# Kernel optimization log

Measured on AMD Instinct MI355X. Metric: run time of the kernel, lower is better.

## Reference

```python
import jax, jax.numpy as jnp
import numpy as np

N_NODES = 10000
N_EDGES = 160000
HIDDEN = 64
NUM_RBF = 32
Q_DIM = 8
CUTOFF_UPPER = 5.0


def silu(x):
    return x * jax.nn.sigmoid(x)


def tensor_norm(X):
    # X: [n, 3, 3, H] -> [n, H] (Frobenius norm squared over the 3x3 dims)
    return (X * X).sum(axis=(1, 2))


def decompose_tensor(X):
    # X: [n, 3, 3, H] -> I: [n, H] (trace/3), A: antisym [n,3,3,H], S: sym traceless [n,3,3,H]
    eye = jnp.eye(3, dtype=X.dtype)[None, :, :, None]
    I = jnp.einsum('naah->nh', X) / 3.0
    Xt = X.transpose(0, 2, 1, 3)
    A = 0.5 * (X - Xt)
    S = 0.5 * (X + Xt) - I[:, None, None, :] * eye
    return I, A, S


def compose_tensor(I, A, S):
    eye = jnp.eye(3, dtype=A.dtype)[None, :, :, None]
    return I[:, None, None, :] * eye + A + S


def tmm(P, Q):
    # 3x3 matmul per (atom, channel): [n,3,3,H] x [n,3,3,H] -> [n,3,3,H]
    return jnp.einsum('nach,ncbh->nabh', P, Q)


def setup_inputs() -> dict:
    key = jax.random.key(0)
    ks = jax.random.split(key, 16)
    H = HIDDEN
    inp = {
        'X': jax.random.normal(ks[0], (N_NODES, 3, 3, H), jnp.float32),
        'charges': jax.random.normal(ks[1], (N_NODES, Q_DIM), jnp.float32),
        'edge_weight': jax.random.uniform(ks[2], (N_EDGES,), jnp.float32) * CUTOFF_UPPER,
        'edge_attr': jax.random.normal(ks[3], (N_EDGES, NUM_RBF), jnp.float32),
        'edge_index': jax.random.randint(ks[4], (2, N_EDGES), 0, N_NODES, jnp.int32),
    }
    d_in = NUM_RBF + 2 * Q_DIM
    inp['Ws1'] = jax.random.normal(ks[5], (d_in, H), jnp.float32) / np.sqrt(d_in).astype(np.float32)
    inp['bs1'] = jnp.zeros((H,), jnp.float32)
    inp['Ws2'] = jax.random.normal(ks[6], (H, 2 * H), jnp.float32) / np.sqrt(H).astype(np.float32)
    inp['bs2'] = jnp.zeros((2 * H,), jnp.float32)
    inp['Ws3'] = jax.random.normal(ks[7], (2 * H, 3 * H), jnp.float32) / np.sqrt(2 * H).astype(np.float32)
    inp['bs3'] = jnp.zeros((3 * H,), jnp.float32)
    for i in range(6):
        inp['Wt%d' % i] = jax.random.normal(ks[8 + i], (H, H), jnp.float32) / np.sqrt(H).astype(np.float32)
    return inp


def reference(X, charges, edge_weight, edge_attr, Ws1, bs1, Ws2, bs2, Ws3, bs3,
              Wt0, Wt1, Wt2, Wt3, Wt4, Wt5, edge_index):
    H = HIDDEN
    n = X.shape[0]
    row, col = edge_index[0], edge_index[1]
    # cosine cutoff (cutoff_lower = 0)
    C = 0.5 * (jnp.cos(edge_weight * (jnp.pi / CUTOFF_UPPER)) + 1.0)
    C = C * (edge_weight < CUTOFF_UPPER).astype(X.dtype)
    # edge scalar MLP on [rbf, q_i, q_j]
    h = jnp.concatenate([edge_attr, charges[row], charges[col]], axis=-1)
    h = silu(h @ Ws1 + bs1)
    h = silu(h @ Ws2 + bs2)
    h = silu(h @ Ws3 + bs3)
    w = (h * C[:, None]).reshape(h.shape[0], 3, H)  # [E, 3, H]
    # normalize node tensors
    X = X / (tensor_norm(X) + 1.0)[:, None, None, :]
    I, A, S = decompose_tensor(X)
    I = I @ Wt0
    A = A @ Wt1
    S = S @ Wt2
    Y = compose_tensor(I, A, S)
    # message passing: gather I/A/S at source (edge_index[1]), weight per component, scatter-add at dest (edge_index[0])
    eye = jnp.eye(3, dtype=X.dtype)[None, :, :, None]
    msg_e = ((w[:, 0] * I[col])[:, None, None, :] * eye
             + w[:, 1][:, None, None, :] * A[col]
             + w[:, 2][:, None, None, :] * S[col])  # [E, 3, 3, H]
    msg = jax.ops.segment_sum(msg_e, row, num_segments=n)  # [n, 3, 3, H]
    # O(3): C = msg @ Y + Y @ msg (3x3 matmul per channel)
    Cm = tmm(msg, Y) + tmm(Y, msg)
    I2, A2, S2 = decompose_tensor(Cm)
    normp1 = tensor_norm(Cm) + 1.0
    I2 = I2 / normp1
    A2 = A2 / normp1[:, None, None, :]
    S2 = S2 / normp1[:, None, None, :]
    I2 = I2 @ Wt3
    A2 = A2 @ Wt4
    S2 = S2 @ Wt5
    dX = compose_tensor(I2, A2, S2)
    return X + dX + tmm(dX, dX)
```

## Files before the change

kernel.cpp:

```cpp
#include <hip/hip_runtime.h>
#include <math.h>

#define HD 64

typedef _Float16 half8 __attribute__((ext_vector_type(8)));
typedef _Float16 half4v __attribute__((ext_vector_type(4)));
typedef float floatx4 __attribute__((ext_vector_type(4)));

__device__ __forceinline__ float silu_f(float x) {
    return x * __builtin_amdgcn_rcpf(1.0f + __expf(-x));
}

__global__ __launch_bounds__(256) void node_pre(
    const float* __restrict__ X,
    const float* __restrict__ Wt0, const float* __restrict__ Wt1, const float* __restrict__ Wt2,
    float* __restrict__ Tn, _Float16* __restrict__ TnH, int N)
{
    int sub = threadIdx.x >> 6;
    int h = threadIdx.x & 63;
    int n = blockIdx.x * 4 + sub;
    int nn = (n < N) ? n : (N - 1);

    const float* Xb = X + (size_t)nn * 9 * HD + h;
    float x[9];
    float nrm = 0.f;
#pragma unroll
    for (int i = 0; i < 9; ++i) { x[i] = Xb[i * HD]; nrm += x[i] * x[i]; }
    float inv = 1.0f / (nrm + 1.0f);
#pragma unroll
    for (int i = 0; i < 9; ++i) x[i] *= inv;

    float I0 = (x[0] + x[4] + x[8]) * (1.0f / 3.0f);
    __shared__ float comp[4][10][HD];
    comp[sub][0][h] = I0;
    comp[sub][1][h] = 0.5f * (x[1] - x[3]);
    comp[sub][2][h] = 0.5f * (x[2] - x[6]);
    comp[sub][3][h] = 0.5f * (x[5] - x[7]);
    comp[sub][4][h] = x[0] - I0;
    comp[sub][5][h] = 0.5f * (x[1] + x[3]);
    comp[sub][6][h] = 0.5f * (x[2] + x[6]);
    comp[sub][7][h] = x[4] - I0;
    comp[sub][8][h] = 0.5f * (x[5] + x[7]);
    comp[sub][9][h] = x[8] - I0;
    __syncthreads();
    float acc[10];
#pragma unroll
    for (int i = 0; i < 10; ++i) acc[i] = 0.f;
    for (int k = 0; k < HD; ++k) {
        float w0 = Wt0[k * HD + h];
        float w1 = Wt1[k * HD + h];
        float w2 = Wt2[k * HD + h];
        acc[0] += comp[sub][0][k] * w0;
        acc[1] += comp[sub][1][k] * w1;
        acc[2] += comp[sub][2][k] * w1;
        acc[3] += comp[sub][3][k] * w1;
#pragma unroll
        for (int j = 0; j < 6; ++j) acc[4 + j] += comp[sub][4 + j][k] * w2;
    }
    if (n < N) {
        float* tp = Tn + (size_t)n * 640 + h;
        _Float16* th = TnH + (size_t)n * 640 + h;
#pragma unroll
        for (int i = 0; i < 10; ++i) {
            tp[i * 64] = acc[i];
            th[i * 64] = (_Float16)acc[i];
        }
    }
}

__global__ __launch_bounds__(256) void count_kernel(
    const int* __restrict__ edge_index, int* __restrict__ cnt, int E)
{
    int e = blockIdx.x * 256 + threadIdx.x;
    if (e < E) atomicAdd(&cnt[edge_index[e]], 1);
}

__global__ __launch_bounds__(1024) void scanA(
    const int* __restrict__ cnt, int* __restrict__ offs, int* __restrict__ partial, int N)
{
    __shared__ int wsum[16];
    int tid = threadIdx.x, wid = tid >> 6, lane = tid & 63;
    int i = blockIdx.x * 1024 + tid;
    int v = (i < N) ? cnt[i] : 0;
    int s = v;
#pragma unroll
    for (int d = 1; d < 64; d <<= 1) {
        int t = __shfl_up(s, d, 64);
        if (lane >= d) s += t;
    }
    if (lane == 63) wsum[wid] = s;
    __syncthreads();
    if (tid == 0) {
        int run = 0;
#pragma unroll
        for (int w = 0; w < 16; ++w) { int t = wsum[w]; wsum[w] = run; run += t; }
        partial[blockIdx.x] = run;
    }
    __syncthreads();
    if (i < N) offs[i] = wsum[wid] + s - v;
}

__global__ __launch_bounds__(64) void scanB(int* __restrict__ partial, int nb)
{
    int lane = threadIdx.x;
    int v = (lane < nb) ? partial[lane] : 0;
    int s = v;
#pragma unroll
    for (int d = 1; d < 64; d <<= 1) {
        int t = __shfl_up(s, d, 64);
        if (lane >= d) s += t;
    }
    if (lane < nb) partial[lane] = s - v;
}

__global__ __launch_bounds__(256) void scanC(
    int* __restrict__ offs, const int* __restrict__ partial, int* __restrict__ curs,
    int N, int E)
{
    int i = blockIdx.x * 256 + threadIdx.x;
    if (i < N) {
        int o = offs[i] + partial[i >> 10];
        offs[i] = o;
        curs[i] = o;
    }
    if (i == 0) offs[N] = E;
}

__global__ __launch_bounds__(256) void place_kernel(
    const int* __restrict__ edge_index, int* __restrict__ curs,
    int* __restrict__ rank, int* __restrict__ colP, int E)
{
    int e = blockIdx.x * 256 + threadIdx.x;
    if (e < E) {
        int p = atomicAdd(&curs[edge_index[e]], 1);
        rank[e] = p;
        colP[p] = edge_index[E + e];
    }
}

__global__ __launch_bounds__(256) void wconv(
    const float* __restrict__ Ws1, const float* __restrict__ Ws2, const float* __restrict__ Ws3,
    _Float16* __restrict__ W1f, _Float16* __restrict__ W2f, _Float16* __restrict__ W3f)
{
    int id = blockIdx.x * 256 + threadIdx.x;
    if (id < 4096) {
        int i = id & 7, l = (id >> 3) & 63, t = id >> 9;
        int s = t >> 2, nt = t & 3;
        int k = s * 32 + (l >> 4) * 8 + i;
        int n = nt * 16 + (l & 15);
        W1f[id] = (k < 48) ? (_Float16)Ws1[k * 64 + n] : (_Float16)0.f;
    } else if (id < 4096 + 8192) {
        int j = id - 4096;
        int i = j & 7, l = (j >> 3) & 63, t = j >> 9;
        int s = t >> 3, nt = t & 7;
        int k = s * 32 + (l >> 4) * 8 + i;
        int n = nt * 16 + (l & 15);
        W2f[j] = (_Float16)Ws2[k * 128 + n];
    } else if (id < 4096 + 8192 + 24576) {
        int j = id - 4096 - 8192;
        int i = j & 7, l = (j >> 3) & 63, t = j >> 9;
        int s = t / 12, nt = t % 12;
        int k = s * 32 + (l >> 4) * 8 + i;
        int n = nt * 16 + (l & 15);
        W3f[j] = (_Float16)Ws3[k * 192 + n];
    }
}

__global__ __launch_bounds__(256, 4) void mlp_mfma(
    const float* __restrict__ edge_attr, const float* __restrict__ charges,
    const float* __restrict__ edge_weight, const int* __restrict__ edge_index,
    const int* __restrict__ rank,
    const _Float16* __restrict__ W1f, const float* __restrict__ bs1,
    const _Float16* __restrict__ W2f, const float* __restrict__ bs2,
    const _Float16* __restrict__ W3f, const float* __restrict__ bs3,
    _Float16* __restrict__ bufH, int E)
{
    __shared__ __align__(16) _Float16 act[4][16][200];
    __shared__ float cvsS[4][16];
    __shared__ int rankSS[4][16];

    int tid = threadIdx.x;
    int wv = tid >> 6, l = tid & 63;
    int base = blockIdx.x * 64 + wv * 16;
    int row16 = l & 15, quad = l >> 4;

#pragma unroll
    for (int i = 0; i < 4; ++i) {
        int slot = l + i * 64;
        int e_l = slot >> 4, f = slot & 15;
        int e = base + e_l;
        int ee = (e < E) ? e : (E - 1);
        float4 v = make_float4(0.f, 0.f, 0.f, 0.f);
        if (f < 8) {
            v = *(const float4*)(edge_attr + (size_t)ee * 32 + f * 4);
        } else if (f < 10) {
            int r = edge_index[ee];
            v = *(const float4*)(charges + (size_t)r * 8 + (f - 8) * 4);
        } else if (f < 12) {
            int c = edge_index[E + ee];
            v = *(const float4*)(charges + (size_t)c * 8 + (f - 10) * 4);
        }
        half4v hv = { (_Float16)v.x, (_Float16)v.y, (_Float16)v.z, (_Float16)v.w };
        *(half4v*)&act[wv][e_l][f * 4] = hv;
    }
    if (l < 16) {
        int e = base + l;
        int ee = (e < E) ? e : (E - 1);
        rankSS[wv][l] = rank[ee];
        float wgt = edge_weight[ee];
        float cv = 0.5f * (__cosf(wgt * 0.6283185307179586f) + 1.0f);
        cvsS[wv][l] = (wgt < 5.0f) ? cv : 0.0f;
    }

    half8 A[4];
    A[0] = *(const half8*)&act[wv][row16][quad * 8];
    A[1] = *(const half8*)&act[wv][row16][32 + quad * 8];
    floatx4 acc1[4];
    {
        half8 W[8];
#pragma unroll
        for (int t = 0; t < 8; ++t)
            W[t] = *(const half8*)(W1f + ((size_t)t * 64 + l) * 8);
#pragma unroll
        for (int nt = 0; nt < 4; ++nt) {
            floatx4 c = {0.f, 0.f, 0.f, 0.f};
            c = __builtin_amdgcn_mfma_f32_16x16x32_f16(A[0], W[nt], c, 0, 0, 0);
            c = __builtin_amdgcn_mfma_f32_16x16x32_f16(A[1], W[4 + nt], c, 0, 0, 0);
            acc1[nt] = c;
        }
    }
#pragma unroll
    for (int nt = 0; nt < 4; ++nt) {
        float b = bs1[nt * 16 + row16];
#pragma unroll
        for (int r = 0; r < 4; ++r)
            act[wv][quad * 4 + r][64 + nt * 16 + row16] = (_Float16)silu_f(acc1[nt][r] + b);
    }

    A[0] = *(const half8*)&act[wv][row16][64 + quad * 8];
    A[1] = *(const half8*)&act[wv][row16][96 + quad * 8];
    floatx4 acc2[8];
#pragma unroll
    for (int nt = 0; nt < 8; ++nt) acc2[nt] = (floatx4){0.f, 0.f, 0.f, 0.f};
#pragma unroll
    for (int s = 0; s < 2; ++s) {
        half8 W[8];
#pragma unroll
        for (int nt = 0; nt < 8; ++nt)
            W[nt] = *(const half8*)(W2f + ((size_t)(s * 8 + nt) * 64 + l) * 8);
#pragma unroll
        for (int nt = 0; nt < 8; ++nt)
            acc2[nt] = __builtin_amdgcn_mfma_f32_16x16x32_f16(A[s], W[nt], acc2[nt], 0, 0, 0);
    }
#pragma unroll
    for (int nt = 0; nt < 8; ++nt) {
        float b = bs2[nt * 16 + row16];
#pragma unroll
        for (int r = 0; r < 4; ++r)
            act[wv][quad * 4 + r][nt * 16 + row16] = (_Float16)silu_f(acc2[nt][r] + b);
    }

    A[0] = *(const half8*)&act[wv][row16][quad * 8];
    A[1] = *(const half8*)&act[wv][row16][32 + quad * 8];
    A[2] = *(const half8*)&act[wv][row16][64 + quad * 8];
    A[3] = *(const half8*)&act[wv][row16][96 + quad * 8];

    float cvrow[4];
#pragma unroll
    for (int r = 0; r < 4; ++r) cvrow[r] = cvsS[wv][quad * 4 + r];

#pragma unroll
    for (int g = 0; g < 2; ++g) {
        floatx4 acc3[6];
#pragma unroll
        for (int j = 0; j < 6; ++j) acc3[j] = (floatx4){0.f, 0.f, 0.f, 0.f};
#pragma unroll
        for (int s = 0; s < 4; ++s) {
            half8 W[6];
#pragma unroll
            for (int j = 0; j < 6; ++j)
                W[j] = *(const half8*)(W3f + ((size_t)(s * 12 + g * 6 + j) * 64 + l) * 8);
#pragma unroll
            for (int j = 0; j < 6; ++j)
                acc3[j] = __builtin_amdgcn_mfma_f32_16x16x32_f16(A[s], W[j], acc3[j], 0, 0, 0);
        }
#pragma unroll
        for (int j = 0; j < 6; ++j) {
            int nt = g * 6 + j;
            float b = bs3[nt * 16 + row16];
#pragma unroll
            for (int r = 0; r < 4; ++r)
                act[wv][quad * 4 + r][nt * 16 + row16] =
                    (_Float16)(silu_f(acc3[j][r] + b) * cvrow[r]);
        }
    }
    {
        int fr = l >> 2;
        int ef = base + fr;
        if (ef < E) {
            _Float16* dst = bufH + (size_t)rankSS[wv][fr] * 192;
#pragma unroll
            for (int i = 0; i < 6; ++i) {
                int j = (l & 3) + i * 4;
                *(half8*)(dst + j * 8) = *(const half8*)&act[wv][fr][j * 8];
            }
        }
    }
}

__global__ __launch_bounds__(256) void msg_kernel(
    const _Float16* __restrict__ bufH, const int* __restrict__ colP,
    const int* __restrict__ offs, const _Float16* __restrict__ TnH,
    float* __restrict__ Mn, int N)
{
    __shared__ float part[2][2][10][64];
    int slot = threadIdx.x >> 7;
    int half = (threadIdx.x >> 6) & 1;
    int lane = threadIdx.x & 63;
    int n = blockIdx.x * 2 + slot;
    int nn = (n < N) ? n : (N - 1);
    int beg = offs[nn], end = offs[nn + 1];
    int mid = beg + ((end - beg + 1) >> 1);
    int s0 = half ? mid : beg;
    int s1 = half ? end : mid;

    float a0 = 0.f, a1 = 0.f, a2 = 0.f, a3 = 0.f, a4 = 0.f;
    float a5 = 0.f, a6 = 0.f, a7 = 0.f, a8 = 0.f, a9 = 0.f;
#pragma unroll 2
    for (int idx = s0; idx < s1; ++idx) {
        int c = colP[idx];
        const _Float16* wp = bufH + (size_t)idx * 192;
        float w0 = (float)wp[lane];
        float w1 = (float)wp[64 + lane];
        float w2 = (float)wp[128 + lane];
        const _Float16* tp = TnH + (size_t)c * 640;
        a0 += w0 * (float)tp[lane];
        a1 += w1 * (float)tp[64 + lane];
        a2 += w1 * (float)tp[128 + lane];
        a3 += w1 * (float)tp[192 + lane];
        a4 += w2 * (float)tp[256 + lane];
        a5 += w2 * (float)tp[320 + lane];
        a6 += w2 * (float)tp[384 + lane];
        a7 += w2 * (float)tp[448 + lane];
        a8 += w2 * (float)tp[512 + lane];
        a9 += w2 * (float)tp[576 + lane];
    }
    part[slot][half][0][lane] = a0; part[slot][half][1][lane] = a1;
    part[slot][half][2][lane] = a2; part[slot][half][3][lane] = a3;
    part[slot][half][4][lane] = a4; part[slot][half][5][lane] = a5;
    part[slot][half][6][lane] = a6; part[slot][half][7][lane] = a7;
    part[slot][half][8][lane] = a8; part[slot][half][9][lane] = a9;
    __syncthreads();

    if (n < N) {
        float* mp = Mn + (size_t)n * 640;
#pragma unroll
        for (int j = 0; j < 5; ++j) {
            int c = half * 5 + j;
            mp[c * 64 + lane] = part[slot][0][c][lane] + part[slot][1][c][lane];
        }
    }
}

__global__ __launch_bounds__(256) void node_post(
    const float* __restrict__ X,
    const float* __restrict__ Tn, const float* __restrict__ Mn,
    const float* __restrict__ Wt3, const float* __restrict__ Wt4, const float* __restrict__ Wt5,
    float* __restrict__ out, int N)
{
    int sub = threadIdx.x >> 6;
    int h = threadIdx.x & 63;
    int n = blockIdx.x * 4 + sub;
    int nn = (n < N) ? n : (N - 1);

    const float* Xb = X + (size_t)nn * 9 * HD + h;
    float x[9];
    float nr = 0.f;
#pragma unroll
    for (int i = 0; i < 9; ++i) { x[i] = Xb[i * HD]; nr += x[i] * x[i]; }
    float xinv = 1.0f / (nr + 1.0f);
#pragma unroll
    for (int i = 0; i < 9; ++i) x[i] *= xinv;

    const float* tp = Tn + (size_t)nn * 640 + h;
    const float* mp = Mn + (size_t)nn * 640 + h;
    float yI = tp[0], mI = mp[0];
    float yA[3], yS[6], mA[3], mS[6];
#pragma unroll
    for (int j = 0; j < 3; ++j) { yA[j] = tp[(1 + j) * 64]; mA[j] = mp[(1 + j) * 64]; }
#pragma unroll
    for (int j = 0; j < 6; ++j) { yS[j] = tp[(4 + j) * 64]; mS[j] = mp[(4 + j) * 64]; }

    float M[3][3] = {
        { mI + mS[0],     mA[0] + mS[1],   mA[1] + mS[2] },
        { -mA[0] + mS[1], mI + mS[3],      mA[2] + mS[4] },
        { -mA[1] + mS[2], -mA[2] + mS[4],  mI + mS[5] } };
    float Y[3][3] = {
        { yI + yS[0],     yA[0] + yS[1],   yA[1] + yS[2] },
        { -yA[0] + yS[1], yI + yS[3],      yA[2] + yS[4] },
        { -yA[1] + yS[2], -yA[2] + yS[4],  yI + yS[5] } };

    float Cm[3][3];
    float nrm = 0.f;
#pragma unroll
    for (int a = 0; a < 3; ++a) {
#pragma unroll
        for (int b = 0; b < 3; ++b) {
            float s = 0.f;
#pragma unroll
            for (int c = 0; c < 3; ++c) s += M[a][c] * Y[c][b] + Y[a][c] * M[c][b];
            Cm[a][b] = s;
            nrm += s * s;
        }
    }
    float inv = 1.0f / (nrm + 1.0f);
    float tr3 = (Cm[0][0] + Cm[1][1] + Cm[2][2]) * (1.0f / 3.0f);

    __shared__ float comp[4][10][HD];
    comp[sub][0][h] = tr3 * inv;
    comp[sub][1][h] = 0.5f * (Cm[0][1] - Cm[1][0]) * inv;
    comp[sub][2][h] = 0.5f * (Cm[0][2] - Cm[2][0]) * inv;
    comp[sub][3][h] = 0.5f * (Cm[1][2] - Cm[2][1]) * inv;
    comp[sub][4][h] = (Cm[0][0] - tr3) * inv;
    comp[sub][5][h] = 0.5f * (Cm[0][1] + Cm[1][0]) * inv;
    comp[sub][6][h] = 0.5f * (Cm[0][2] + Cm[2][0]) * inv;
    comp[sub][7][h] = (Cm[1][1] - tr3) * inv;
    comp[sub][8][h] = 0.5f * (Cm[1][2] + Cm[2][1]) * inv;
    comp[sub][9][h] = (Cm[2][2] - tr3) * inv;
    __syncthreads();

    float acc[10];
#pragma unroll
    for (int i = 0; i < 10; ++i) acc[i] = 0.f;
    for (int k = 0; k < HD; ++k) {
        float w3 = Wt3[k * HD + h];
        float w4 = Wt4[k * HD + h];
        float w5 = Wt5[k * HD + h];
        acc[0] += comp[sub][0][k] * w3;
        acc[1] += comp[sub][1][k] * w4;
        acc[2] += comp[sub][2][k] * w4;
        acc[3] += comp[sub][3][k] * w4;
#pragma unroll
        for (int j = 0; j < 6; ++j) acc[4 + j] += comp[sub][4 + j][k] * w5;
    }
    float D[3][3] = {
        { acc[0] + acc[4],  acc[1] + acc[5],  acc[2] + acc[6] },
        { -acc[1] + acc[5], acc[0] + acc[7],  acc[3] + acc[8] },
        { -acc[2] + acc[6], -acc[3] + acc[8], acc[0] + acc[9] } };

    if (n < N) {
        float* ob = out + (size_t)n * 9 * HD + h;
#pragma unroll
        for (int a = 0; a < 3; ++a) {
#pragma unroll
            for (int b = 0; b < 3; ++b) {
                float s = 0.f;
#pragma unroll
                for (int c = 0; c < 3; ++c) s += D[a][c] * D[c][b];
                ob[(a * 3 + b) * HD] = x[a * 3 + b] + D[a][b] + s;
            }
        }
    }
}

extern "C" void kernel_launch(void* const* d_in, const int* in_sizes, int n_in,
                              void* d_out, int out_size, void* d_ws, size_t ws_size,
                              hipStream_t stream)
{
    const float* X           = (const float*)d_in[0];
    const float* charges     = (const float*)d_in[1];
    const float* edge_weight = (const float*)d_in[2];
    const float* edge_attr   = (const float*)d_in[3];
    const int*   edge_index  = (const int*)d_in[4];
    const float* Ws1 = (const float*)d_in[5];
    const float* bs1 = (const float*)d_in[6];
    const float* Ws2 = (const float*)d_in[7];
    const float* bs2 = (const float*)d_in[8];
    const float* Ws3 = (const float*)d_in[9];
    const float* bs3 = (const float*)d_in[10];
    const float* Wt0 = (const float*)d_in[11];
    const float* Wt1 = (const float*)d_in[12];
    const float* Wt2 = (const float*)d_in[13];
    const float* Wt3 = (const float*)d_in[14];
    const float* Wt4 = (const float*)d_in[15];
    const float* Wt5 = (const float*)d_in[16];

    int N = in_sizes[0] / (9 * HD);
    int E = in_sizes[2];

    float* ws = (float*)d_ws;
    float* Tn  = ws;
    float* Mn  = Tn + (size_t)N * 640;
    _Float16* TnH  = (_Float16*)(Mn + (size_t)N * 640);
    _Float16* bufH = TnH + (size_t)N * 640;
    int* cnt   = (int*)(bufH + (size_t)E * 192);
    int* offs  = cnt + N;
    int* curs  = offs + N + 1;
    int* rank  = curs + N;
    int* colP  = rank + E;
    int* partial = colP + E;
    size_t fofs = ((size_t)((char*)(partial + 64) - (char*)d_ws) + 15) & ~(size_t)15;
    _Float16* W1f = (_Float16*)((char*)d_ws + fofs);
    _Float16* W2f = W1f + 4096;
    _Float16* W3f = W2f + 8192;

    hipMemsetAsync(cnt, 0, (size_t)N * sizeof(int), stream);

    int nbE256 = (E + 255) / 256;
    int nbN1024 = (N + 1023) / 1024;
    count_kernel<<<nbE256, 256, 0, stream>>>(edge_index, cnt, E);
    scanA<<<nbN1024, 1024, 0, stream>>>(cnt, offs, partial, N);
    scanB<<<1, 64, 0, stream>>>(partial, nbN1024);
    scanC<<<(N + 255) / 256, 256, 0, stream>>>(offs, partial, curs, N, E);
    place_kernel<<<nbE256, 256, 0, stream>>>(edge_index, curs, rank, colP, E);

    wconv<<<144, 256, 0, stream>>>(Ws1, Ws2, Ws3, W1f, W2f, W3f);

    node_pre<<<(N + 3) / 4, 256, 0, stream>>>(X, Wt0, Wt1, Wt2, Tn, TnH, N);

    int nbE64 = (E + 63) / 64;
    mlp_mfma<<<nbE64, 256, 0, stream>>>(edge_attr, charges, edge_weight, edge_index,
                                        rank, W1f, bs1, W2f, bs2, W3f, bs3, bufH, E);

    msg_kernel<<<(N + 1) / 2, 256, 0, stream>>>(bufH, colP, offs, TnH, Mn, N);

    node_post<<<(N + 3) / 4, 256, 0, stream>>>(X, Tn, Mn, Wt3, Wt4, Wt5, (float*)d_out, N);
}
```

Baseline: 178.8 us.

## Merge small launches and cut MLP register and shared-memory footprint

Folds the weight-conversion kernel into the node preprocessing launch as extra blocks, and drops the scanB launch by having scanC sum the preceding block partials itself. In the edge MLP, the third layer is split into three 64-column chunks, each written out before the next, so the shared activation buffer shrinks from 200 to 136 halves per row and fewer accumulators stay live. Launch bounds are raised to target 8 blocks per CU. The aim is fewer launch gaps and higher occupancy, at the cost of an extra store pass and possible register pressure or spills under the tighter bound.

```diff
diff --git a/kernel.cpp b/kernel.cpp
--- a/kernel.cpp
+++ b/kernel.cpp
@@ -11,11 +11,39 @@
     return x * __builtin_amdgcn_rcpf(1.0f + __expf(-x));
 }
 
-__global__ __launch_bounds__(256) void node_pre(
+__global__ __launch_bounds__(256) void pre_wconv(
     const float* __restrict__ X,
     const float* __restrict__ Wt0, const float* __restrict__ Wt1, const float* __restrict__ Wt2,
-    float* __restrict__ Tn, _Float16* __restrict__ TnH, int N)
-{
+    float* __restrict__ Tn, _Float16* __restrict__ TnH, int N, int nbPre,
+    const float* __restrict__ Ws1, const float* __restrict__ Ws2, const float* __restrict__ Ws3,
+    _Float16* __restrict__ W1f, _Float16* __restrict__ W2f, _Float16* __restrict__ W3f)
+{
+    if (blockIdx.x >= nbPre) {
+        int id = (blockIdx.x - nbPre) * 256 + threadIdx.x;
+        if (id < 4096) {
+            int i = id & 7, l = (id >> 3) & 63, t = id >> 9;
+            int s = t >> 2, nt = t & 3;
+            int k = s * 32 + (l >> 4) * 8 + i;
+            int n = nt * 16 + (l & 15);
+            W1f[id] = (k < 48) ? (_Float16)Ws1[k * 64 + n] : (_Float16)0.f;
+        } else if (id < 4096 + 8192) {
+            int j = id - 4096;
+            int i = j & 7, l = (j >> 3) & 63, t = j >> 9;
+            int s = t >> 3, nt = t & 7;
+            int k = s * 32 + (l >> 4) * 8 + i;
+            int n = nt * 16 + (l & 15);
+            W2f[j] = (_Float16)Ws2[k * 128 + n];
+        } else if (id < 4096 + 8192 + 24576) {
+            int j = id - 4096 - 8192;
+            int i = j & 7, l = (j >> 3) & 63, t = j >> 9;
+            int s = t / 12, nt = t % 12;
+            int k = s * 32 + (l >> 4) * 8 + i;
+            int n = nt * 16 + (l & 15);
+            W3f[j] = (_Float16)Ws3[k * 192 + n];
+        }
+        return;
+    }
+
     int sub = threadIdx.x >> 6;
     int h = threadIdx.x & 63;
     int n = blockIdx.x * 4 + sub;
@@ -100,26 +128,16 @@
     if (i < N) offs[i] = wsum[wid] + s - v;
 }
 
-__global__ __launch_bounds__(64) void scanB(int* __restrict__ partial, int nb)
-{
-    int lane = threadIdx.x;
-    int v = (lane < nb) ? partial[lane] : 0;
-    int s = v;
-#pragma unroll
-    for (int d = 1; d < 64; d <<= 1) {
-        int t = __shfl_up(s, d, 64);
-        if (lane >= d) s += t;
-    }
-    if (lane < nb) partial[lane] = s - v;
-}
-
 __global__ __launch_bounds__(256) void scanC(
     int* __restrict__ offs, const int* __restrict__ partial, int* __restrict__ curs,
     int N, int E)
 {
     int i = blockIdx.x * 256 + threadIdx.x;
     if (i < N) {
-        int o = offs[i] + partial[i >> 10];
+        int b = i >> 10;
+        int basev = 0;
+        for (int w = 0; w < b; ++w) basev += partial[w];
+        int o = offs[i] + basev;
         offs[i] = o;
         curs[i] = o;
     }
@@ -138,35 +156,7 @@
     }
 }
 
-__global__ __launch_bounds__(256) void wconv(
-    const float* __restrict__ Ws1, const float* __restrict__ Ws2, const float* __restrict__ Ws3,
-    _Float16* __restrict__ W1f, _Float16* __restrict__ W2f, _Float16* __restrict__ W3f)
-{
-    int id = blockIdx.x * 256 + threadIdx.x;
-    if (id < 4096) {
-        int i = id & 7, l = (id >> 3) & 63, t = id >> 9;
-        int s = t >> 2, nt = t & 3;
-        int k = s * 32 + (l >> 4) * 8 + i;
-        int n = nt * 16 + (l & 15);
-        W1f[id] = (k < 48) ? (_Float16)Ws1[k * 64 + n] : (_Float16)0.f;
-    } else if (id < 4096 + 8192) {
-        int j = id - 4096;
-        int i = j & 7, l = (j >> 3) & 63, t = j >> 9;
-        int s = t >> 3, nt = t & 7;
-        int k = s * 32 + (l >> 4) * 8 + i;
-        int n = nt * 16 + (l & 15);
-        W2f[j] = (_Float16)Ws2[k * 128 + n];
-    } else if (id < 4096 + 8192 + 24576) {
-        int j = id - 4096 - 8192;
-        int i = j & 7, l = (j >> 3) & 63, t = j >> 9;
-        int s = t / 12, nt = t % 12;
-        int k = s * 32 + (l >> 4) * 8 + i;
-        int n = nt * 16 + (l & 15);
-        W3f[j] = (_Float16)Ws3[k * 192 + n];
-    }
-}
-
-__global__ __launch_bounds__(256, 4) void mlp_mfma(
+__global__ __launch_bounds__(256, 8) void mlp_mfma(
     const float* __restrict__ edge_attr, const float* __restrict__ charges,
     const float* __restrict__ edge_weight, const int* __restrict__ edge_index,
     const int* __restrict__ rank,
@@ -175,7 +165,7 @@
     const _Float16* __restrict__ W3f, const float* __restrict__ bs3,
     _Float16* __restrict__ bufH, int E)
 {
-    __shared__ __align__(16) _Float16 act[4][16][200];
+    __shared__ __align__(16) _Float16 act[4][16][136];
     __shared__ float cvsS[4][16];
     __shared__ int rankSS[4][16];
 
@@ -212,15 +202,15 @@
         cvsS[wv][l] = (wgt < 5.0f) ? cv : 0.0f;
     }
 
-    half8 A[4];
+    half8 A[2];
     A[0] = *(const half8*)&act[wv][row16][quad * 8];
     A[1] = *(const half8*)&act[wv][row16][32 + quad * 8];
-    floatx4 acc1[4];
     {
         half8 W[8];
 #pragma unroll
         for (int t = 0; t < 8; ++t)
             W[t] = *(const half8*)(W1f + ((size_t)t * 64 + l) * 8);
+        floatx4 acc1[4];
 #pragma unroll
         for (int nt = 0; nt < 4; ++nt) {
             floatx4 c = {0.f, 0.f, 0.f, 0.f};
@@ -228,42 +218,44 @@
             c = __builtin_amdgcn_mfma_f32_16x16x32_f16(A[1], W[4 + nt], c, 0, 0, 0);
             acc1[nt] = c;
         }
-    }
-#pragma unroll
-    for (int nt = 0; nt < 4; ++nt) {
-        float b = bs1[nt * 16 + row16];
-#pragma unroll
-        for (int r = 0; r < 4; ++r)
-            act[wv][quad * 4 + r][64 + nt * 16 + row16] = (_Float16)silu_f(acc1[nt][r] + b);
+#pragma unroll
+        for (int nt = 0; nt < 4; ++nt) {
+            float b = bs1[nt * 16 + row16];
+#pragma unroll
+            for (int r = 0; r < 4; ++r)
+                act[wv][quad * 4 + r][64 + nt * 16 + row16] = (_Float16)silu_f(acc1[nt][r] + b);
+        }
     }
 
     A[0] = *(const half8*)&act[wv][row16][64 + quad * 8];
     A[1] = *(const half8*)&act[wv][row16][96 + quad * 8];
-    floatx4 acc2[8];
-#pragma unroll
-    for (int nt = 0; nt < 8; ++nt) acc2[nt] = (floatx4){0.f, 0.f, 0.f, 0.f};
-#pragma unroll
-    for (int s = 0; s < 2; ++s) {
-        half8 W[8];
-#pragma unroll
-        for (int nt = 0; nt < 8; ++nt)
-            W[nt] = *(const half8*)(W2f + ((size_t)(s * 8 + nt) * 64 + l) * 8);
-#pragma unroll
-        for (int nt = 0; nt < 8; ++nt)
-            acc2[nt] = __builtin_amdgcn_mfma_f32_16x16x32_f16(A[s], W[nt], acc2[nt], 0, 0, 0);
-    }
-#pragma unroll
-    for (int nt = 0; nt < 8; ++nt) {
-        float b = bs2[nt * 16 + row16];
-#pragma unroll
-        for (int r = 0; r < 4; ++r)
-            act[wv][quad * 4 + r][nt * 16 + row16] = (_Float16)silu_f(acc2[nt][r] + b);
-    }
-
-    A[0] = *(const half8*)&act[wv][row16][quad * 8];
-    A[1] = *(const half8*)&act[wv][row16][32 + quad * 8];
-    A[2] = *(const half8*)&act[wv][row16][64 + quad * 8];
-    A[3] = *(const half8*)&act[wv][row16][96 + quad * 8];
+    {
+        floatx4 acc2[8];
+#pragma unroll
+        for (int nt = 0; nt < 8; ++nt) acc2[nt] = (floatx4){0.f, 0.f, 0.f, 0.f};
+#pragma unroll
+        for (int s = 0; s < 2; ++s) {
+            half8 W[8];
+#pragma unroll
+            for (int nt = 0; nt < 8; ++nt)
+                W[nt] = *(const half8*)(W2f + ((size_t)(s * 8 + nt) * 64 + l) * 8);
+#pragma unroll
+            for (int nt = 0; nt < 8; ++nt)
+                acc2[nt] = __builtin_amdgcn_mfma_f32_16x16x32_f16(A[s], W[nt], acc2[nt], 0, 0, 0);
+        }
+#pragma unroll
+        for (int nt = 0; nt < 8; ++nt) {
+            float b = bs2[nt * 16 + row16];
+#pragma unroll
+            for (int r = 0; r < 4; ++r)
+                act[wv][quad * 4 + r][nt * 16 + row16] = (_Float16)silu_f(acc2[nt][r] + b);
+        }
+    }
+
+    half8 A3[4];
+#pragma unroll
+    for (int s = 0; s < 4; ++s)
+        A3[s] = *(const half8*)&act[wv][row16][s * 32 + quad * 8];
 
     float cvrow[4];
 #pragma unroll
@@ -271,27 +263,27 @@
 
 #pragma unroll
     for (int g = 0; g < 2; ++g) {
-        floatx4 acc3[6];
-#pragma unroll
-        for (int j = 0; j < 6; ++j) acc3[j] = (floatx4){0.f, 0.f, 0.f, 0.f};
+        floatx4 acc[4];
+#pragma unroll
+        for (int j = 0; j < 4; ++j) acc[j] = (floatx4){0.f, 0.f, 0.f, 0.f};
 #pragma unroll
         for (int s = 0; s < 4; ++s) {
-            half8 W[6];
-#pragma unroll
-            for (int j = 0; j < 6; ++j)
-                W[j] = *(const half8*)(W3f + ((size_t)(s * 12 + g * 6 + j) * 64 + l) * 8);
-#pragma unroll
-            for (int j = 0; j < 6; ++j)
-                acc3[j] = __builtin_amdgcn_mfma_f32_16x16x32_f16(A[s], W[j], acc3[j], 0, 0, 0);
-        }
-#pragma unroll
-        for (int j = 0; j < 6; ++j) {
-            int nt = g * 6 + j;
+            half8 W[4];
+#pragma unroll
+            for (int j = 0; j < 4; ++j)
+                W[j] = *(const half8*)(W3f + ((size_t)(s * 12 + g * 4 + j) * 64 + l) * 8);
+#pragma unroll
+            for (int j = 0; j < 4; ++j)
+                acc[j] = __builtin_amdgcn_mfma_f32_16x16x32_f16(A3[s], W[j], acc[j], 0, 0, 0);
+        }
+#pragma unroll
+        for (int j = 0; j < 4; ++j) {
+            int nt = g * 4 + j;
             float b = bs3[nt * 16 + row16];
 #pragma unroll
             for (int r = 0; r < 4; ++r)
                 act[wv][quad * 4 + r][nt * 16 + row16] =
-                    (_Float16)(silu_f(acc3[j][r] + b) * cvrow[r]);
+                    (_Float16)(silu_f(acc[j][r] + b) * cvrow[r]);
         }
     }
     {
@@ -300,9 +292,44 @@
         if (ef < E) {
             _Float16* dst = bufH + (size_t)rankSS[wv][fr] * 192;
 #pragma unroll
-            for (int i = 0; i < 6; ++i) {
+            for (int i = 0; i < 4; ++i) {
                 int j = (l & 3) + i * 4;
                 *(half8*)(dst + j * 8) = *(const half8*)&act[wv][fr][j * 8];
+            }
+        }
+    }
+    {
+        floatx4 acc[4];
+#pragma unroll
+        for (int j = 0; j < 4; ++j) acc[j] = (floatx4){0.f, 0.f, 0.f, 0.f};
+#pragma unroll
+        for (int s = 0; s < 4; ++s) {
+            half8 W[4];
+#pragma unroll
+            for (int j = 0; j < 4; ++j)
+                W[j] = *(const half8*)(W3f + ((size_t)(s * 12 + 8 + j) * 64 + l) * 8);
+#pragma unroll
+            for (int j = 0; j < 4; ++j)
+                acc[j] = __builtin_amdgcn_mfma_f32_16x16x32_f16(A3[s], W[j], acc[j], 0, 0, 0);
+        }
+#pragma unroll
+        for (int j = 0; j < 4; ++j) {
+            float b = bs3[(8 + j) * 16 + row16];
+#pragma unroll
+            for (int r = 0; r < 4; ++r)
+                act[wv][quad * 4 + r][j * 16 + row16] =
+                    (_Float16)(silu_f(acc[j][r] + b) * cvrow[r]);
+        }
+    }
+    {
+        int fr = l >> 2;
+        int ef = base + fr;
+        if (ef < E) {
+            _Float16* dst = bufH + (size_t)rankSS[wv][fr] * 192;
+#pragma unroll
+            for (int i = 0; i < 2; ++i) {
+                int j = (l & 3) + i * 4;
+                *(half8*)(dst + (16 + j) * 8) = *(const half8*)&act[wv][fr][j * 8];
             }
         }
     }
@@ -510,13 +537,12 @@
     int nbN1024 = (N + 1023) / 1024;
     count_kernel<<<nbE256, 256, 0, stream>>>(edge_index, cnt, E);
     scanA<<<nbN1024, 1024, 0, stream>>>(cnt, offs, partial, N);
-    scanB<<<1, 64, 0, stream>>>(partial, nbN1024);
     scanC<<<(N + 255) / 256, 256, 0, stream>>>(offs, partial, curs, N, E);
     place_kernel<<<nbE256, 256, 0, stream>>>(edge_index, curs, rank, colP, E);
 
-    wconv<<<144, 256, 0, stream>>>(Ws1, Ws2, Ws3, W1f, W2f, W3f);
-
-    node_pre<<<(N + 3) / 4, 256, 0, stream>>>(X, Wt0, Wt1, Wt2, Tn, TnH, N);
+    int nbPre = (N + 3) / 4;
+    pre_wconv<<<nbPre + 144, 256, 0, stream>>>(X, Wt0, Wt1, Wt2, Tn, TnH, N, nbPre,
+                                               Ws1, Ws2, Ws3, W1f, W2f, W3f);
 
     int nbE64 = (E + 63) / 64;
     mlp_mfma<<<nbE64, 256, 0, stream>>>(edge_attr, charges, edge_weight, edge_index,
```

Measured after the change: 180.3 us. About the same (+0.8%).
